# Performance work log

Hardware: AMD Instinct MI355X
Metric: run time of the kernel (lower is better)

Reference implementation:

```python
import jax, jax.numpy as jnp
import numpy as np

N = 2000
E = 128
H = 8
DH = E // H
K = 32  # max_neighbors
CLAMP = 1e4


def _sanitize(t):
    t = jnp.nan_to_num(t, nan=0.0, posinf=CLAMP, neginf=-CLAMP)
    return jnp.clip(t, -CLAMP, CLAMP)


def _layernorm(h, g, b, eps=1e-5):
    mu = h.mean(-1, keepdims=True)
    var = ((h - mu) ** 2).mean(-1, keepdims=True)
    return (h - mu) * jax.lax.rsqrt(var + eps) * g + b


def setup_inputs() -> dict:
    key = jax.random.key(0)
    ks = jax.random.split(key, 8)
    x = jax.random.normal(ks[0], (N, E), dtype=jnp.float32)
    coords9 = jax.random.normal(ks[1], (N, 9), dtype=jnp.float32)
    prompt_signal = jax.random.normal(ks[2], (E,), dtype=jnp.float32)
    pe_w = jax.random.normal(ks[3], (3, 32), dtype=jnp.float32) / np.sqrt(3.0)
    pe_b = jnp.zeros((32,), jnp.float32)
    pe_g = jnp.ones((32,), jnp.float32)
    pe_bt = jnp.zeros((32,), jnp.float32)
    in_w = jax.random.normal(ks[4], (3 * E, E), dtype=jnp.float32) / np.sqrt(E)
    in_b = jnp.zeros((3 * E,), jnp.float32)
    out_w = jax.random.normal(ks[5], (E, E), dtype=jnp.float32) / np.sqrt(E)
    out_b = jnp.zeros((E,), jnp.float32)
    return {"x": x, "coords9": coords9, "prompt_signal": prompt_signal,
            "pe_w": pe_w, "pe_b": pe_b, "pe_g": pe_g, "pe_bt": pe_bt,
            "in_w": in_w, "in_b": in_b, "out_w": out_w, "out_b": out_b}


def reference(x, coords9, prompt_signal, pe_w, pe_b, pe_g, pe_bt, in_w, in_b, out_w, out_b):
    n = x.shape[0]
    verts = coords9.reshape(n, 3, 3)
    cent = verts.mean(axis=1)  # (N,3)

    # pairwise centroid distances (only geo-relation channel that affects the output;
    # cos_angles/area_ratios/boundary_sharing feed geo_bias which is dead code in forward)
    diff = cent[:, None, :] - cent[None, :, :]
    dist = jnp.sqrt(jnp.sum(diff * diff, axis=-1) + 1e-20)  # (N,N)

    # positional encoder: Linear(3,32) -> GELU(exact) -> LayerNorm(32)
    pe = jax.nn.gelu(cent @ pe_w + pe_b, approximate=False)
    pe = _layernorm(pe, pe_g, pe_bt)  # (N,32)

    prompt_enhanced = x + prompt_signal[None, :]
    pos_enhanced = jnp.concatenate([prompt_enhanced[:, : 3 * E // 4], pe], axis=-1)  # (N,128)

    # top-K nearest neighbors -> additive attention mask (0 for kept, -inf-like otherwise)
    _, topk_idx = jax.lax.top_k(-dist, K)  # (N,K) smallest distances
    big_neg = jnp.float32(-1e9)
    attn_mask = jnp.full((n, n), big_neg, dtype=jnp.float32)
    attn_mask = attn_mask.at[jnp.arange(n)[:, None], topk_idx].set(0.0)

    # nn.MultiheadAttention (self-attention, eval mode -> no dropout)
    qkv = pos_enhanced @ in_w.T + in_b  # (N,3E)
    q, k, v = jnp.split(qkv, 3, axis=-1)
    q = q.reshape(n, H, DH).transpose(1, 0, 2)  # (H,N,DH)
    k = k.reshape(n, H, DH).transpose(1, 0, 2)
    v = v.reshape(n, H, DH).transpose(1, 0, 2)
    scores = jnp.einsum('hnd,hmd->hnm', q, k) / np.sqrt(DH) + attn_mask[None]
    probs = jax.nn.softmax(scores, axis=-1)
    o = jnp.einsum('hnm,hmd->hnd', probs, v)  # (H,N,DH)
    o = o.transpose(1, 0, 2).reshape(n, E)
    out = o @ out_w.T + out_b
    return _sanitize(out)
```

## Files before the change

### kernel.cpp

```cpp
#include <hip/hip_runtime.h>
#include <math.h>

#define N_NODES 2000
#define E_DIM   128
#define QKV_W   384

__global__ __launch_bounds__(256) void prep_kernel(
    const float* __restrict__ x, const float* __restrict__ coords9,
    const float* __restrict__ ps, const float* __restrict__ pe_w,
    const float* __restrict__ pe_b, const float* __restrict__ pe_g,
    const float* __restrict__ pe_bt,
    float* __restrict__ cent, float* __restrict__ pos)
{
    int tid = threadIdx.x;
    int g = tid >> 5, lane = tid & 31;
    int row = blockIdx.x * 8 + g;

    const float* c9 = coords9 + row * 9;
    float cx = (c9[0] + c9[3] + c9[6]) * (1.0f / 3.0f);
    float cy = (c9[1] + c9[4] + c9[7]) * (1.0f / 3.0f);
    float cz = (c9[2] + c9[5] + c9[8]) * (1.0f / 3.0f);
    if (lane < 3) cent[row * 3 + lane] = (lane == 0) ? cx : ((lane == 1) ? cy : cz);

    #pragma unroll
    for (int k = 0; k < 3; ++k) {
        int c = lane + 32 * k;
        pos[row * E_DIM + c] = x[row * E_DIM + c] + ps[c];
    }

    int j = lane;
    float h = cx * pe_w[j] + cy * pe_w[32 + j] + cz * pe_w[64 + j] + pe_b[j];
    float ge = 0.5f * h * (1.0f + erff(h * 0.7071067811865476f));
    float s = ge;
    #pragma unroll
    for (int m = 16; m >= 1; m >>= 1) s += __shfl_xor(s, m);
    float mu = s * (1.0f / 32.0f);
    float d = ge - mu;
    float v = d * d;
    #pragma unroll
    for (int m = 16; m >= 1; m >>= 1) v += __shfl_xor(v, m);
    float var = v * (1.0f / 32.0f);
    float y = d * (1.0f / sqrtf(var + 1e-5f)) * pe_g[j] + pe_bt[j];
    pos[row * E_DIM + 96 + j] = y;
}

__global__ __launch_bounds__(256) void qkv_kernel(
    const float* __restrict__ pos, const float* __restrict__ in_w,
    const float* __restrict__ in_b, float* __restrict__ qkv)
{
    __shared__ __align__(16) float As[128 * 32];
    int tid = threadIdx.x;
    int rt = blockIdx.x / 3, ct = blockIdx.x % 3;
    int rbase = rt * 32, cbase = ct * 128;

    {
        int r = tid & 31, e0 = (tid >> 5) * 16;
        int row = rbase + r;
        #pragma unroll
        for (int q = 0; q < 4; ++q) {
            int e = e0 + q * 4;
            float4 vv = (row < N_NODES) ? *(const float4*)&pos[row * E_DIM + e]
                                        : make_float4(0.f, 0.f, 0.f, 0.f);
            As[(e + 0) * 32 + r] = vv.x;
            As[(e + 1) * 32 + r] = vv.y;
            As[(e + 2) * 32 + r] = vv.z;
            As[(e + 3) * 32 + r] = vv.w;
        }
    }
    __syncthreads();

    int cg = tid & 31, rg = tid >> 5;
    int c0 = cbase + cg * 4, r0 = rg * 4;
    float acc[4][4];
    #pragma unroll
    for (int i = 0; i < 4; ++i)
        #pragma unroll
        for (int jj = 0; jj < 4; ++jj) acc[i][jj] = 0.f;

    for (int k0 = 0; k0 < 128; k0 += 4) {
        float4 a0 = *(const float4*)&As[(k0 + 0) * 32 + r0];
        float4 a1 = *(const float4*)&As[(k0 + 1) * 32 + r0];
        float4 a2 = *(const float4*)&As[(k0 + 2) * 32 + r0];
        float4 a3 = *(const float4*)&As[(k0 + 3) * 32 + r0];
        #pragma unroll
        for (int ci = 0; ci < 4; ++ci) {
            float4 b = *(const float4*)&in_w[(c0 + ci) * E_DIM + k0];
            acc[0][ci] += a0.x * b.x + a1.x * b.y + a2.x * b.z + a3.x * b.w;
            acc[1][ci] += a0.y * b.x + a1.y * b.y + a2.y * b.z + a3.y * b.w;
            acc[2][ci] += a0.z * b.x + a1.z * b.y + a2.z * b.z + a3.z * b.w;
            acc[3][ci] += a0.w * b.x + a1.w * b.y + a2.w * b.z + a3.w * b.w;
        }
    }

    #pragma unroll
    for (int ri = 0; ri < 4; ++ri) {
        int row = rbase + r0 + ri;
        if (row < N_NODES) {
            float4 o4;
            o4.x = acc[ri][0] + in_b[c0 + 0];
            o4.y = acc[ri][1] + in_b[c0 + 1];
            o4.z = acc[ri][2] + in_b[c0 + 2];
            o4.w = acc[ri][3] + in_b[c0 + 3];
            *(float4*)&qkv[row * QKV_W + c0] = o4;
        }
    }
}

__global__ __launch_bounds__(256) void attn_kernel(
    const float* __restrict__ cent, const float* __restrict__ qkv,
    float* __restrict__ o_out)
{
    __shared__ unsigned int hist[256];
    __shared__ int sh_bmin, sh_nless, sh_sel, sh_eq;
    __shared__ unsigned int sh_prefix;
    __shared__ int waveSum[4];
    __shared__ int topk[32];
    __shared__ int eqIdx[256];
    __shared__ __align__(16) float qs[128];
    __shared__ float pr[256];

    int tid = threadIdx.x;
    int row = blockIdx.x;
    int lane = tid & 63, wid = tid >> 6;

    float cix = cent[row * 3 + 0], ciy = cent[row * 3 + 1], ciz = cent[row * 3 + 2];
    unsigned int kbits[8];
    bool valid[8];
    {
        #pragma clang fp contract(off)
        #pragma unroll
        for (int l = 0; l < 8; ++l) {
            int j = tid + 256 * l;
            valid[l] = (j < N_NODES);
            float key = __int_as_float(0x7f800000);
            if (valid[l]) {
                float dx = cix - cent[j * 3 + 0];
                float dy = ciy - cent[j * 3 + 1];
                float dz = ciz - cent[j * 3 + 2];
                float a = dx * dx;
                float b = dy * dy;
                float c = dz * dz;
                float d2 = ((a + b) + c) + 1e-20f;
                key = sqrtf(d2);
            }
            kbits[l] = __float_as_uint(key);
        }
    }

    if (tid == 0) { sh_prefix = 0u; sh_nless = 0; sh_sel = 0; sh_eq = 0; }

    for (int level = 0; level < 4; ++level) {
        hist[tid] = 0u;
        if (tid == 0) sh_bmin = 256;
        __syncthreads();
        unsigned int pref = sh_prefix;
        int nless = sh_nless;
        int shift = 24 - 8 * level;
        #pragma unroll
        for (int l = 0; l < 8; ++l) {
            if (valid[l]) {
                unsigned int kb = kbits[l];
                bool match = (level == 0) || ((kb >> (shift + 8)) == pref);
                if (match) atomicAdd(&hist[(kb >> shift) & 255u], 1u);
            }
        }
        __syncthreads();
        int h = (int)hist[tid];
        int incl = h;
        #pragma unroll
        for (int dd = 1; dd < 64; dd <<= 1) {
            int u = __shfl_up(incl, dd);
            if (lane >= dd) incl += u;
        }
        if (lane == 63) waveSum[wid] = incl;
        __syncthreads();
        int off = 0;
        for (int w = 0; w < wid; ++w) off += waveSum[w];
        int cum = incl + off;
        int need = 32 - nless;
        if (cum >= need && (cum - h) < need) atomicMin(&sh_bmin, tid);
        __syncthreads();
        if (tid == sh_bmin) {
            sh_prefix = (pref << 8) | (unsigned int)tid;
            sh_nless = nless + (cum - h);
        }
        __syncthreads();
    }

    unsigned int T = sh_prefix;
    int req = 32 - sh_nless;

    #pragma unroll
    for (int l = 0; l < 8; ++l) {
        if (valid[l]) {
            unsigned int kb = kbits[l];
            int j = tid + 256 * l;
            if (kb < T) {
                int p = atomicAdd(&sh_sel, 1);
                topk[p] = j;
            } else if (kb == T) {
                int e = atomicAdd(&sh_eq, 1);
                if (e < 256) eqIdx[e] = j;
            }
        }
    }
    if (tid < 128) qs[tid] = qkv[row * QKV_W + tid];
    __syncthreads();
    int eq = min(sh_eq, 256);
    if (tid < eq) {
        int my = eqIdx[tid];
        int rank = 0;
        for (int u = 0; u < eq; ++u) rank += (eqIdx[u] < my) ? 1 : 0;
        if (rank < req) {
            int p = atomicAdd(&sh_sel, 1);
            topk[p] = my;
        }
    }
    __syncthreads();

    {
        int h = tid >> 5, j = tid & 31;
        int jj = topk[j];
        const float4* kp = (const float4*)&qkv[jj * QKV_W + 128 + h * 16];
        const float4* qp = (const float4*)&qs[h * 16];
        float s = 0.f;
        #pragma unroll
        for (int i = 0; i < 4; ++i) {
            float4 kv = kp[i], qv = qp[i];
            s += qv.x * kv.x + qv.y * kv.y + qv.z * kv.z + qv.w * kv.w;
        }
        s *= 0.25f;
        float m = s;
        #pragma unroll
        for (int msk = 16; msk >= 1; msk >>= 1) m = fmaxf(m, __shfl_xor(m, msk));
        float p = expf(s - m);
        float su = p;
        #pragma unroll
        for (int msk = 16; msk >= 1; msk >>= 1) su += __shfl_xor(su, msk);
        pr[tid] = p / su;
    }
    __syncthreads();

    if (tid < 128) {
        int h = tid >> 4;
        float acc = 0.f;
        #pragma unroll
        for (int j = 0; j < 32; ++j) {
            int jj = topk[j];
            acc += pr[h * 32 + j] * qkv[jj * QKV_W + 256 + tid];
        }
        o_out[row * E_DIM + tid] = acc;
    }
}

__device__ __forceinline__ float sanitize(float v)
{
    v = (v == v) ? v : 0.f;
    return fminf(fmaxf(v, -1e4f), 1e4f);
}

__global__ __launch_bounds__(256) void proj_kernel(
    const float* __restrict__ o_in, const float* __restrict__ out_w,
    const float* __restrict__ out_b, float* __restrict__ out)
{
    __shared__ __align__(16) float Os[128 * 16];
    int tid = threadIdx.x;
    int rbase = blockIdx.x * 16;

    {
        int r = tid & 15, e0 = (tid >> 4) * 8;
        #pragma unroll
        for (int q = 0; q < 2; ++q) {
            int e = e0 + q * 4;
            float4 vv = *(const float4*)&o_in[(rbase + r) * E_DIM + e];
            Os[(e + 0) * 16 + r] = vv.x;
            Os[(e + 1) * 16 + r] = vv.y;
            Os[(e + 2) * 16 + r] = vv.z;
            Os[(e + 3) * 16 + r] = vv.w;
        }
    }
    __syncthreads();

    int cg = tid & 31, rg = tid >> 5;
    int c0 = cg * 4, r0 = rg * 2;
    float acc[2][4];
    #pragma unroll
    for (int i = 0; i < 2; ++i)
        #pragma unroll
        for (int jj = 0; jj < 4; ++jj) acc[i][jj] = 0.f;

    for (int k0 = 0; k0 < 128; k0 += 4) {
        float2 a0 = *(const float2*)&Os[(k0 + 0) * 16 + r0];
        float2 a1 = *(const float2*)&Os[(k0 + 1) * 16 + r0];
        float2 a2 = *(const float2*)&Os[(k0 + 2) * 16 + r0];
        float2 a3 = *(const float2*)&Os[(k0 + 3) * 16 + r0];
        #pragma unroll
        for (int ci = 0; ci < 4; ++ci) {
            float4 b = *(const float4*)&out_w[(c0 + ci) * E_DIM + k0];
            acc[0][ci] += a0.x * b.x + a1.x * b.y + a2.x * b.z + a3.x * b.w;
            acc[1][ci] += a0.y * b.x + a1.y * b.y + a2.y * b.z + a3.y * b.w;
        }
    }

    #pragma unroll
    for (int ri = 0; ri < 2; ++ri) {
        int row = rbase + r0 + ri;
        float4 o4;
        o4.x = sanitize(acc[ri][0] + out_b[c0 + 0]);
        o4.y = sanitize(acc[ri][1] + out_b[c0 + 1]);
        o4.z = sanitize(acc[ri][2] + out_b[c0 + 2]);
        o4.w = sanitize(acc[ri][3] + out_b[c0 + 3]);
        *(float4*)&out[row * E_DIM + c0] = o4;
    }
}

extern "C" void kernel_launch(void* const* d_in, const int* in_sizes, int n_in,
                              void* d_out, int out_size, void* d_ws, size_t ws_size,
                              hipStream_t stream)
{
    const float* x      = (const float*)d_in[0];
    const float* coords = (const float*)d_in[1];
    const float* ps     = (const float*)d_in[2];
    const float* pe_w   = (const float*)d_in[3];
    const float* pe_b   = (const float*)d_in[4];
    const float* pe_g   = (const float*)d_in[5];
    const float* pe_bt  = (const float*)d_in[6];
    const float* in_w   = (const float*)d_in[7];
    const float* in_b   = (const float*)d_in[8];
    const float* out_w  = (const float*)d_in[9];
    const float* out_b  = (const float*)d_in[10];
    float* out = (float*)d_out;

    float* ws   = (float*)d_ws;
    float* cent = ws;
    float* pos  = ws + 6016;
    float* qkvb = ws + 6016 + 256000;
    float* ob   = ws + 6016 + 256000 + 768000;

    prep_kernel<<<250, 256, 0, stream>>>(x, coords, ps, pe_w, pe_b, pe_g, pe_bt, cent, pos);
    qkv_kernel<<<189, 256, 0, stream>>>(pos, in_w, in_b, qkvb);
    attn_kernel<<<2000, 256, 0, stream>>>(cent, qkvb, ob);
    proj_kernel<<<125, 256, 0, stream>>>(ob, out_w, out_b, out);
}
```

Baseline: 137.8 us.

## Replace 4-pass radix top-k select with single value-range histogram pass

Swaps the four-level 8-bit radix select on distance bits for one 256-bin histogram over the row's min-max distance range, found with a block min/max reduction. Candidates in the threshold bin are ranked by exact key and then index. This cuts the histogram/scan/sync passes from four to one. The risk is heavy crowding in the boundary bin: clustered distances can push more than 256 elements into it, and the eqIdx cap then truncates candidates and can select wrong neighbours. The pairwise rank loop over that bin is quadratic.

New measurement: 124.1 us. 1.11x faster.

```diff
diff --git a/kernel.cpp b/kernel.cpp
--- a/kernel.cpp
+++ b/kernel.cpp
@@ -111,11 +111,13 @@
     float* __restrict__ o_out)
 {
     __shared__ unsigned int hist[256];
-    __shared__ int sh_bmin, sh_nless, sh_sel, sh_eq;
-    __shared__ unsigned int sh_prefix;
+    __shared__ float wMin[4], wMax[4];
+    __shared__ float sh_lo, sh_scale;
+    __shared__ int sh_b, sh_nless, sh_sel, sh_eq;
     __shared__ int waveSum[4];
     __shared__ int topk[32];
     __shared__ int eqIdx[256];
+    __shared__ unsigned int eqKey[256];
     __shared__ __align__(16) float qs[128];
     __shared__ float pr[256];
 
@@ -126,6 +128,8 @@
     float cix = cent[row * 3 + 0], ciy = cent[row * 3 + 1], ciz = cent[row * 3 + 2];
     unsigned int kbits[8];
     bool valid[8];
+    float lmin = __int_as_float(0x7f800000);
+    float lmax = __int_as_float(0xff800000);
     {
         #pragma clang fp contract(off)
         #pragma unroll
@@ -142,87 +146,103 @@
                 float c = dz * dz;
                 float d2 = ((a + b) + c) + 1e-20f;
                 key = sqrtf(d2);
+                lmin = fminf(lmin, key);
+                lmax = fmaxf(lmax, key);
             }
             kbits[l] = __float_as_uint(key);
         }
     }
 
-    if (tid == 0) { sh_prefix = 0u; sh_nless = 0; sh_sel = 0; sh_eq = 0; }
-
-    for (int level = 0; level < 4; ++level) {
-        hist[tid] = 0u;
-        if (tid == 0) sh_bmin = 256;
-        __syncthreads();
-        unsigned int pref = sh_prefix;
-        int nless = sh_nless;
-        int shift = 24 - 8 * level;
-        #pragma unroll
-        for (int l = 0; l < 8; ++l) {
-            if (valid[l]) {
-                unsigned int kb = kbits[l];
-                bool match = (level == 0) || ((kb >> (shift + 8)) == pref);
-                if (match) atomicAdd(&hist[(kb >> shift) & 255u], 1u);
-            }
-        }
-        __syncthreads();
-        int h = (int)hist[tid];
-        int incl = h;
-        #pragma unroll
-        for (int dd = 1; dd < 64; dd <<= 1) {
-            int u = __shfl_up(incl, dd);
-            if (lane >= dd) incl += u;
-        }
-        if (lane == 63) waveSum[wid] = incl;
-        __syncthreads();
-        int off = 0;
-        for (int w = 0; w < wid; ++w) off += waveSum[w];
-        int cum = incl + off;
-        int need = 32 - nless;
-        if (cum >= need && (cum - h) < need) atomicMin(&sh_bmin, tid);
-        __syncthreads();
-        if (tid == sh_bmin) {
-            sh_prefix = (pref << 8) | (unsigned int)tid;
-            sh_nless = nless + (cum - h);
-        }
-        __syncthreads();
-    }
-
-    unsigned int T = sh_prefix;
-    int req = 32 - sh_nless;
+    #pragma unroll
+    for (int m = 32; m >= 1; m >>= 1) {
+        lmin = fminf(lmin, __shfl_xor(lmin, m));
+        lmax = fmaxf(lmax, __shfl_xor(lmax, m));
+    }
+    if (lane == 0) { wMin[wid] = lmin; wMax[wid] = lmax; }
+    hist[tid] = 0u;
+    if (tid == 0) { sh_sel = 0; sh_eq = 0; }
+    __syncthreads();
+    if (tid == 0) {
+        float lo = fminf(fminf(wMin[0], wMin[1]), fminf(wMin[2], wMin[3]));
+        float hi = fmaxf(fmaxf(wMax[0], wMax[1]), fmaxf(wMax[2], wMax[3]));
+        sh_lo = lo;
+        sh_scale = 255.0f / fmaxf(hi - lo, 1e-30f);
+    }
+    __syncthreads();
+    float lo = sh_lo, scale = sh_scale;
 
     #pragma unroll
     for (int l = 0; l < 8; ++l) {
         if (valid[l]) {
-            unsigned int kb = kbits[l];
+            float key = __uint_as_float(kbits[l]);
+            int bin = (int)((key - lo) * scale);
+            bin = min(max(bin, 0), 255);
+            atomicAdd(&hist[bin], 1u);
+        }
+    }
+    __syncthreads();
+
+    int h = (int)hist[tid];
+    int incl = h;
+    #pragma unroll
+    for (int dd = 1; dd < 64; dd <<= 1) {
+        int u = __shfl_up(incl, dd);
+        if (lane >= dd) incl += u;
+    }
+    if (lane == 63) waveSum[wid] = incl;
+    __syncthreads();
+    int off = 0;
+    for (int w = 0; w < wid; ++w) off += waveSum[w];
+    int cum = incl + off;
+    if (cum >= 32 && (cum - h) < 32) {
+        sh_b = tid;
+        sh_nless = cum - h;
+    }
+    __syncthreads();
+
+    int b = sh_b;
+    int req = 32 - sh_nless;
+
+    #pragma unroll
+    for (int l = 0; l < 8; ++l) {
+        if (valid[l]) {
+            float key = __uint_as_float(kbits[l]);
+            int bin = (int)((key - lo) * scale);
+            bin = min(max(bin, 0), 255);
             int j = tid + 256 * l;
-            if (kb < T) {
+            if (bin < b) {
                 int p = atomicAdd(&sh_sel, 1);
                 topk[p] = j;
-            } else if (kb == T) {
+            } else if (bin == b) {
                 int e = atomicAdd(&sh_eq, 1);
-                if (e < 256) eqIdx[e] = j;
+                if (e < 256) { eqIdx[e] = j; eqKey[e] = kbits[l]; }
             }
         }
     }
     if (tid < 128) qs[tid] = qkv[row * QKV_W + tid];
     __syncthreads();
+
     int eq = min(sh_eq, 256);
     if (tid < eq) {
-        int my = eqIdx[tid];
+        int myIdx = eqIdx[tid];
+        unsigned int myKey = eqKey[tid];
         int rank = 0;
-        for (int u = 0; u < eq; ++u) rank += (eqIdx[u] < my) ? 1 : 0;
+        for (int u = 0; u < eq; ++u) {
+            unsigned int ku = eqKey[u];
+            rank += (ku < myKey || (ku == myKey && eqIdx[u] < myIdx)) ? 1 : 0;
+        }
         if (rank < req) {
             int p = atomicAdd(&sh_sel, 1);
-            topk[p] = my;
+            topk[p] = myIdx;
         }
     }
     __syncthreads();
 
     {
-        int h = tid >> 5, j = tid & 31;
+        int hh = tid >> 5, j = tid & 31;
         int jj = topk[j];
-        const float4* kp = (const float4*)&qkv[jj * QKV_W + 128 + h * 16];
-        const float4* qp = (const float4*)&qs[h * 16];
+        const float4* kp = (const float4*)&qkv[jj * QKV_W + 128 + hh * 16];
+        const float4* qp = (const float4*)&qs[hh * 16];
         float s = 0.f;
         #pragma unroll
         for (int i = 0; i < 4; ++i) {
@@ -242,12 +262,12 @@
     __syncthreads();
 
     if (tid < 128) {
-        int h = tid >> 4;
+        int hh = tid >> 4;
         float acc = 0.f;
         #pragma unroll
         for (int j = 0; j < 32; ++j) {
             int jj = topk[j];
-            acc += pr[h * 32 + j] * qkv[jj * QKV_W + 256 + tid];
+            acc += pr[hh * 32 + j] * qkv[jj * QKV_W + 256 + tid];
         }
         o_out[row * E_DIM + tid] = acc;
     }
```
